# Kernel tuning notes

Measured on AMD Instinct MI355X. Metric: run time of the kernel, lower is better.

The kernel has to match this reference:

```python
import jax, jax.numpy as jnp
import numpy as np

N = 100000   # nodes
DEG = 16     # neighbors per node (uniform CSR)
E = N * DEG  # edges
D = 64       # node feature dim
COORD = 2    # coord_dim used for attention
EPS = 1e-9


def setup_inputs() -> dict:
    key = jax.random.key(0)
    k1, k2, k3, k4 = jax.random.split(key, 4)
    y = jax.random.normal(k1, (N, D), dtype=jnp.float32)
    indices = jax.random.randint(k2, (E,), 0, N, dtype=jnp.int64)
    indptr = (jnp.arange(N + 1, dtype=jnp.int64) * DEG)
    W1 = jax.random.normal(k3, (2 * D, 128), dtype=jnp.float32) * (1.0 / np.sqrt(2 * D))
    b1 = jnp.zeros((128,), dtype=jnp.float32)
    W2 = jax.random.normal(k4, (128, 64), dtype=jnp.float32) * (1.0 / np.sqrt(128))
    b2 = jnp.zeros((64,), dtype=jnp.float32)
    return {"y": y, "indices": indices, "indptr": indptr,
            "W1": W1, "b1": b1, "W2": W2, "b2": b2}


def _csr_repeat_ids(indptr, num_edges):
    # segids[e] = i such that indptr[i] <= e < indptr[i+1]
    return jnp.searchsorted(indptr, jnp.arange(num_edges, dtype=indptr.dtype), side='right') - 1


def _segment_softmax(s, segids, nsegs):
    smax = jax.ops.segment_max(s, segids, num_segments=nsegs)
    e = jnp.exp(s - smax[segids])
    denom = jax.ops.segment_sum(e, segids, num_segments=nsegs)
    return e / denom[segids]


def reference(y, indices, indptr, W1, b1, W2, b2):
    nsegs = y.shape[0]
    num_edges = indices.shape[0]
    segids = _csr_repeat_ids(indptr, num_edges)       # [E]

    rep_y = y[indices]                                # neighbor gather  [E, D]
    self_x = y[segids]                                # == repeat(x, num_reps) since x is y  [E, D]

    # cosine attention on coordinate slice
    qx = self_x[:, :COORD]
    ky = rep_y[:, :COORD]
    qn = qx / jnp.clip(jnp.linalg.norm(qx, axis=-1, keepdims=True), EPS)
    kn = ky / jnp.clip(jnp.linalg.norm(ky, axis=-1, keepdims=True), EPS)
    s = jnp.sum(qn * kn, axis=-1)                     # [E]
    a = _segment_softmax(s, segids, nsegs)            # [E]

    agg = jnp.concatenate([rep_y, self_x], axis=-1)   # [E, 2D]
    h = jax.nn.relu(agg @ W1 + b1)                    # [E, 128]
    m = h @ W2 + b2                                   # [E, 64]

    m = m * a[:, None]
    out = jax.ops.segment_sum(m, segids, num_segments=nsegs)  # [N, 64]
    return out
```

## Files before the change

### kernel.cpp

```cpp
#include <hip/hip_runtime.h>
#include <cstdint>

#define DEG 16
#define NNODE 100000
#define NTILE 3125
#define NT64 1563

typedef _Float16 f16;
typedef _Float16 h2v  __attribute__((ext_vector_type(2)));
typedef _Float16 f16x8 __attribute__((ext_vector_type(8)));
typedef float    f32x4 __attribute__((ext_vector_type(4)));

union U4 { uint4 u; h2v h[4]; f16x8 v; };
union U1 { uint32_t i; h2v h; };

__device__ __forceinline__ h2v pk2h(float a, float b) {
    auto r = __builtin_amdgcn_cvt_pkrtz(a, b);
    h2v o;
    __builtin_memcpy(&o, &r, sizeof(o));
    return o;
}

__device__ __host__ __forceinline__ int kperm(int p) {
    return (p & 0xC3) | ((p & 0x0C) << 2) | ((p & 0x30) >> 2);
}

__global__ __launch_bounds__(256) void k_prep(
    const float* __restrict__ W1, const float* __restrict__ W2,
    f16* __restrict__ W1A, f16* __restrict__ W2A)
{
    const int g0 = blockIdx.x * 256 + threadIdx.x;
    for (int i = g0; i < 16384 + 8192; i += 24 * 256) {
        if (i < 16384) {
            const int j = i & 7, lane = (i >> 3) & 63, kb = (i >> 9) & 1, mt = i >> 10;
            const int m = 16 * mt + (lane & 15);
            const int k = kb * 32 + (lane >> 4) * 8 + j;
            const int row = (m < 128) ? k : (64 + k);
            const int col = m & 127;
            W1A[i] = (f16)W1[row * 128 + col];
        } else {
            const int ii = i - 16384;
            const int j = ii & 7, lane = (ii >> 3) & 63, kb = (ii >> 9) & 3, mt = ii >> 11;
            const int c = 16 * mt + (lane & 15);
            const int p = kb * 32 + (lane >> 4) * 8 + j;
            W2A[ii] = (f16)W2[kperm(p) * 64 + c];
        }
    }
}

__global__ __launch_bounds__(256, 4) void k_uv(
    const float* __restrict__ y, const f16* __restrict__ W1A,
    const float* __restrict__ b1,
    unsigned char* __restrict__ U8, f16* __restrict__ Vh, float2* __restrict__ QN)
{
    __shared__ float ysh[4096];
    const int t = threadIdx.x;
    const long nbase = (long)blockIdx.x * 64;
    const int lane = t & 63;
    const int w = t >> 6;
    const int c16 = lane & 15, q = lane >> 4;

    {
        const size_t max4 = (size_t)NNODE * 16;
        char* yb = (char*)ysh;
        #pragma unroll
        for (int i = 0; i < 4; ++i) {
            const int e = t + i * 256;
            size_t gidx = (size_t)blockIdx.x * 1024 + e;
            if (gidx >= max4) gidx = max4 - 1;
            const float4 v = ((const float4*)y)[gidx];
            const int B = e * 16;
            const int row = B >> 8;
            *(float4*)(yb + (B ^ ((row & 7) << 4))) = v;
        }
    }

    if (QN != nullptr && t < 64) {
        const long node = nbase + t;
        if (node < NNODE) {
            const float qx = y[node * 64], qy = y[node * 64 + 1];
            const float n = fmaxf(sqrtf(qx * qx + qy * qy), 1e-9f);
            QN[node] = make_float2(qx / n, qy / n);
        }
    }
    __syncthreads();

    const char* yb = (const char*)ysh;
    f16x8 bf[4][2];
    #pragma unroll
    for (int nt = 0; nt < 4; ++nt) {
        const int r = 16 * nt + c16;
        const int sw = (r & 7) << 4;
        #pragma unroll
        for (int kb = 0; kb < 2; ++kb) {
            const int base = r * 256 + kb * 128 + q * 32;
            const float4 a = *(const float4*)(yb + (base ^ sw));
            const float4 b = *(const float4*)(yb + ((base + 16) ^ sw));
            U4 rg;
            rg.h[0] = pk2h(a.x, a.y);
            rg.h[1] = pk2h(a.z, a.w);
            rg.h[2] = pk2h(b.x, b.y);
            rg.h[3] = pk2h(b.z, b.w);
            bf[nt][kb] = rg.v;
        }
    }

    f32x4 acc[4][4];
    #pragma unroll
    for (int i = 0; i < 4; ++i)
        #pragma unroll
        for (int nt = 0; nt < 4; ++nt)
            acc[i][nt] = (f32x4){0.f, 0.f, 0.f, 0.f};

    #pragma unroll
    for (int i = 0; i < 4; ++i) {
        const int mt = 4 * w + i;
        #pragma unroll
        for (int kb = 0; kb < 2; ++kb) {
            const f16x8 af = *(const f16x8*)&W1A[((mt * 2 + kb) * 64 + lane) * 8];
            #pragma unroll
            for (int nt = 0; nt < 4; ++nt)
                acc[i][nt] = __builtin_amdgcn_mfma_f32_16x16x32_f16(af, bf[nt][kb], acc[i][nt], 0, 0, 0);
        }
    }

    const bool isV = (w >= 2);
    const int wef = w & 1;
    float4 b1v[4];
    #pragma unroll
    for (int i = 0; i < 4; ++i) b1v[i] = make_float4(0.f, 0.f, 0.f, 0.f);
    if (isV) {
        #pragma unroll
        for (int i = 0; i < 4; ++i)
            b1v[i] = *(const float4*)&b1[wef * 64 + 16 * i + 4 * q];
    }

    #pragma unroll
    for (int nt = 0; nt < 4; ++nt) {
        const long node = nbase + 16 * nt + c16;
        if (node >= NNODE) continue;
        if (!isV) {
            uint4 pkt;
            uint32_t wd[4];
            #pragma unroll
            for (int i = 0; i < 4; ++i) {
                uint32_t v0 = __builtin_amdgcn_cvt_pk_fp8_f32(acc[i][nt][0], acc[i][nt][1], 0, false);
                wd[i] = __builtin_amdgcn_cvt_pk_fp8_f32(acc[i][nt][2], acc[i][nt][3], v0, true);
            }
            pkt.x = wd[0]; pkt.y = wd[1]; pkt.z = wd[2]; pkt.w = wd[3];
            *(uint4*)(U8 + node * 128 + wef * 64 + q * 16) = pkt;
        } else {
            f16* dst = Vh + node * 128 + wef * 64 + q * 16;
            U4 p0, p1;
            p0.h[0] = pk2h(acc[0][nt][0] + b1v[0].x, acc[0][nt][1] + b1v[0].y);
            p0.h[1] = pk2h(acc[0][nt][2] + b1v[0].z, acc[0][nt][3] + b1v[0].w);
            p0.h[2] = pk2h(acc[1][nt][0] + b1v[1].x, acc[1][nt][1] + b1v[1].y);
            p0.h[3] = pk2h(acc[1][nt][2] + b1v[1].z, acc[1][nt][3] + b1v[1].w);
            p1.h[0] = pk2h(acc[2][nt][0] + b1v[2].x, acc[2][nt][1] + b1v[2].y);
            p1.h[1] = pk2h(acc[2][nt][2] + b1v[2].z, acc[2][nt][3] + b1v[2].w);
            p1.h[2] = pk2h(acc[3][nt][0] + b1v[3].x, acc[3][nt][1] + b1v[3].y);
            p1.h[3] = pk2h(acc[3][nt][2] + b1v[3].z, acc[3][nt][3] + b1v[3].w);
            *(uint4*)dst       = p0.u;
            *(uint4*)(dst + 8) = p1.u;
        }
    }
}

template<bool USE_QN>
__global__ __launch_bounds__(256, 6) void k_agg(
    const float* __restrict__ y, const int* __restrict__ idx,
    const unsigned char* __restrict__ U8, const f16* __restrict__ Vh,
    const float2* __restrict__ QN, const f16* __restrict__ W2A,
    const float* __restrict__ b2, float* __restrict__ out)
{
    __shared__ uint32_t accs[8192];

    const int t = threadIdx.x, lane = t & 63, wave = t >> 6;
    const int c16 = lane & 15, quarter = lane >> 4;
    const int nodeBase = blockIdx.x * 32 + wave * 8;

    int jA[8];
    #pragma unroll
    for (int g = 0; g < 8; ++g)
        jA[g] = idx[(nodeBase + g) * DEG + c16];

    float aA[8];
    #pragma unroll
    for (int g = 0; g < 8; ++g) {
        const int i = nodeBase + g;
        float s;
        if (USE_QN) {
            const float2 qn = QN[i];
            const float2 kn = QN[jA[g]];
            s = qn.x * kn.x + qn.y * kn.y;
        } else {
            const float2 qv = *(const float2*)&y[(long)i * 64];
            const float2 kv = *(const float2*)&y[(long)jA[g] * 64];
            const float nq = fmaxf(sqrtf(qv.x * qv.x + qv.y * qv.y), 1e-9f);
            const float nk = fmaxf(sqrtf(kv.x * kv.x + kv.y * kv.y), 1e-9f);
            s = (qv.x * kv.x + qv.y * kv.y) / (nq * nk);
        }
        float m = s;
        #pragma unroll
        for (int d = 1; d < 16; d <<= 1) m = fmaxf(m, __shfl_xor(m, d));
        const float ex = __expf(s - m);
        float sum = ex;
        #pragma unroll
        for (int d = 1; d < 16; d <<= 1) sum += __shfl_xor(sum, d);
        aA[g] = ex / sum;
    }

    const uint2* Uv = (const uint2*)U8;
    const uint4* Vv = (const uint4*)Vh;
    char* accb = (char*)accs;
    char* const myTile = accb + quarter * 8192;

    uint2 ub[2][4];
    U4 vb[2];
    vb[0].u = Vv[(long)nodeBase * 16 + c16];
    #pragma unroll
    for (int ee = 0; ee < 4; ++ee) {
        const long je = __shfl(jA[0], 4 * ee + quarter);
        ub[0][ee] = Uv[je * 16 + c16];
    }

    #pragma unroll
    for (int g = 0; g < 8; ++g) {
        const int cur = g & 1, nx = cur ^ 1;
        if (g < 7) {
            vb[nx].u = Vv[(long)(nodeBase + g + 1) * 16 + c16];
            #pragma unroll
            for (int ee = 0; ee < 4; ++ee) {
                const long je = __shfl(jA[g + 1], 4 * ee + quarter);
                ub[nx][ee] = Uv[je * 16 + c16];
            }
        }
        const h2v z2 = {0, 0};
        h2v r0 = {0, 0}, r1 = {0, 0}, r2 = {0, 0}, r3 = {0, 0};
        #pragma unroll
        for (int ee = 0; ee < 4; ++ee) {
            const float ae = __shfl(aA[g], 4 * ee + quarter);
            const h2v az = pk2h(ae, ae);
            const uint2 uu = ub[cur][ee];
            auto q01 = __builtin_amdgcn_cvt_pk_f32_fp8(uu.x, false);
            auto q23 = __builtin_amdgcn_cvt_pk_f32_fp8(uu.x, true);
            auto q45 = __builtin_amdgcn_cvt_pk_f32_fp8(uu.y, false);
            auto q67 = __builtin_amdgcn_cvt_pk_f32_fp8(uu.y, true);
            const h2v u0 = pk2h(q01[0], q01[1]);
            const h2v u1 = pk2h(q23[0], q23[1]);
            const h2v u2 = pk2h(q45[0], q45[1]);
            const h2v u3 = pk2h(q67[0], q67[1]);
            r0 += __builtin_elementwise_max(u0 + vb[cur].h[0], z2) * az;
            r1 += __builtin_elementwise_max(u1 + vb[cur].h[1], z2) * az;
            r2 += __builtin_elementwise_max(u2 + vb[cur].h[2], z2) * az;
            r3 += __builtin_elementwise_max(u3 + vb[cur].h[3], z2) * az;
        }
        const int rrow = wave * 8 + g;
        U4 pk; pk.h[0] = r0; pk.h[1] = r1; pk.h[2] = r2; pk.h[3] = r3;
        *(uint4*)(myTile + ((rrow * 256 + c16 * 16) ^ ((rrow & 7) << 4))) = pk.u;
    }
    __syncthreads();

    f16x8 waf[4];
    #pragma unroll
    for (int kb = 0; kb < 4; ++kb)
        waf[kb] = *(const f16x8*)&W2A[((wave * 4 + kb) * 64 + lane) * 8];
    const float4 b2v = *(const float4*)&b2[16 * wave + quarter * 4];

    f32x4 d[2];
    #pragma unroll
    for (int nt = 0; nt < 2; ++nt) d[nt] = (f32x4){0.f, 0.f, 0.f, 0.f};
    #pragma unroll
    for (int nt = 0; nt < 2; ++nt) {
        const int n = 16 * nt + c16;
        const int sw = (n & 7) << 4;
        #pragma unroll
        for (int qt = 0; qt < 4; ++qt) {
            #pragma unroll
            for (int kb = 0; kb < 4; ++kb) {
                const f16x8 bfr = *(const f16x8*)(accb + qt * 8192 + ((n * 256 + kb * 64 + quarter * 16) ^ sw));
                d[nt] = __builtin_amdgcn_mfma_f32_16x16x32_f16(waf[kb], bfr, d[nt], 0, 0, 0);
            }
        }
    }
    #pragma unroll
    for (int nt = 0; nt < 2; ++nt) {
        const long node = blockIdx.x * 32 + 16 * nt + c16;
        const int col = 16 * wave + quarter * 4;
        float4 o;
        o.x = d[nt][0] + b2v.x; o.y = d[nt][1] + b2v.y;
        o.z = d[nt][2] + b2v.z; o.w = d[nt][3] + b2v.w;
        *(float4*)&out[node * 64 + col] = o;
    }
}

extern "C" void kernel_launch(void* const* d_in, const int* in_sizes, int n_in,
                              void* d_out, int out_size, void* d_ws, size_t ws_size,
                              hipStream_t stream) {
    const float* y   = (const float*)d_in[0];
    const int*   idx = (const int*)d_in[1];
    const float* W1  = (const float*)d_in[3];
    const float* b1  = (const float*)d_in[4];
    const float* W2  = (const float*)d_in[5];
    const float* b2  = (const float*)d_in[6];
    float* out = (float*)d_out;

    char* ws = (char*)d_ws;
    unsigned char* U8 = (unsigned char*)ws;
    f16* Vh  = (f16*)(ws + 12800000);
    f16* W1A = (f16*)(ws + 38400000);
    f16* W2A = (f16*)(ws + 38432768);
    const size_t qn_off = 38449152;
    const bool useQN = (ws_size >= qn_off + (size_t)NNODE * sizeof(float2));
    float2* QN = useQN ? (float2*)(ws + qn_off) : nullptr;

    k_prep<<<24, 256, 0, stream>>>(W1, W2, W1A, W2A);
    k_uv<<<NT64, 256, 0, stream>>>(y, W1A, b1, U8, Vh, QN);
    if (useQN)
        k_agg<true><<<NTILE, 256, 0, stream>>>(y, idx, U8, Vh, QN, W2A, b2, out);
    else
        k_agg<false><<<NTILE, 256, 0, stream>>>(y, idx, U8, Vh, nullptr, W2A, b2, out);
}
```

Before: 66.99 us.

## Reduce per-edge partials across lanes with shuffles instead of four LDS tiles

Each lane now loads 16 fp8 bytes of the U row (8 lanes per row, 8 edges per pass) instead of 8 bytes. The per-quarter partial sums are reduced within the wave using xor-shuffles before a single LDS tile is written. This shrinks shared memory from 32KB to 8KB and cuts the second-stage MFMA loop from 16 to 4 per tile, which may allow higher occupancy and fewer LDS reads. In exchange it adds 24 shuffles per node group and an extra fp16 summation order, which changes rounding.

```diff
diff --git a/kernel.cpp b/kernel.cpp
--- a/kernel.cpp
+++ b/kernel.cpp
@@ -173,10 +173,12 @@
     const float2* __restrict__ QN, const f16* __restrict__ W2A,
     const float* __restrict__ b2, float* __restrict__ out)
 {
-    __shared__ uint32_t accs[8192];
+    __shared__ uint32_t accs[2048];
 
     const int t = threadIdx.x, lane = t & 63, wave = t >> 6;
     const int c16 = lane & 15, quarter = lane >> 4;
+    const int G = lane >> 3;
+    const int c8 = lane & 7;
     const int nodeBase = blockIdx.x * 32 + wave * 8;
 
     int jA[8];
@@ -210,54 +212,80 @@
         aA[g] = ex / sum;
     }
 
-    const uint2* Uv = (const uint2*)U8;
+    const uint4* Uv = (const uint4*)U8;
     const uint4* Vv = (const uint4*)Vh;
     char* accb = (char*)accs;
-    char* const myTile = accb + quarter * 8192;
-
-    uint2 ub[2][4];
-    U4 vb[2];
-    vb[0].u = Vv[(long)nodeBase * 16 + c16];
-    #pragma unroll
-    for (int ee = 0; ee < 4; ++ee) {
-        const long je = __shfl(jA[0], 4 * ee + quarter);
-        ub[0][ee] = Uv[je * 16 + c16];
-    }
+
+    uint4 ub[2][2], vb[2][2];
+    #pragma unroll
+    for (int ee = 0; ee < 2; ++ee) {
+        const long je = __shfl(jA[0], 8 * ee + G);
+        ub[0][ee] = Uv[je * 8 + c8];
+    }
+    vb[0][0] = Vv[(long)nodeBase * 16 + c8 * 2];
+    vb[0][1] = Vv[(long)nodeBase * 16 + c8 * 2 + 1];
 
     #pragma unroll
     for (int g = 0; g < 8; ++g) {
         const int cur = g & 1, nx = cur ^ 1;
         if (g < 7) {
-            vb[nx].u = Vv[(long)(nodeBase + g + 1) * 16 + c16];
             #pragma unroll
-            for (int ee = 0; ee < 4; ++ee) {
-                const long je = __shfl(jA[g + 1], 4 * ee + quarter);
-                ub[nx][ee] = Uv[je * 16 + c16];
+            for (int ee = 0; ee < 2; ++ee) {
+                const long je = __shfl(jA[g + 1], 8 * ee + G);
+                ub[nx][ee] = Uv[je * 8 + c8];
             }
+            vb[nx][0] = Vv[(long)(nodeBase + g + 1) * 16 + c8 * 2];
+            vb[nx][1] = Vv[(long)(nodeBase + g + 1) * 16 + c8 * 2 + 1];
+        }
+        h2v vh[8];
+        {
+            U4 tv;
+            tv.u = vb[cur][0];
+            vh[0] = tv.h[0]; vh[1] = tv.h[1]; vh[2] = tv.h[2]; vh[3] = tv.h[3];
+            tv.u = vb[cur][1];
+            vh[4] = tv.h[0]; vh[5] = tv.h[1]; vh[6] = tv.h[2]; vh[7] = tv.h[3];
         }
         const h2v z2 = {0, 0};
-        h2v r0 = {0, 0}, r1 = {0, 0}, r2 = {0, 0}, r3 = {0, 0};
-        #pragma unroll
-        for (int ee = 0; ee < 4; ++ee) {
-            const float ae = __shfl(aA[g], 4 * ee + quarter);
+        h2v r[8] = {z2, z2, z2, z2, z2, z2, z2, z2};
+        #pragma unroll
+        for (int ee = 0; ee < 2; ++ee) {
+            const float ae = __shfl(aA[g], 8 * ee + G);
             const h2v az = pk2h(ae, ae);
-            const uint2 uu = ub[cur][ee];
-            auto q01 = __builtin_amdgcn_cvt_pk_f32_fp8(uu.x, false);
-            auto q23 = __builtin_amdgcn_cvt_pk_f32_fp8(uu.x, true);
-            auto q45 = __builtin_amdgcn_cvt_pk_f32_fp8(uu.y, false);
-            auto q67 = __builtin_amdgcn_cvt_pk_f32_fp8(uu.y, true);
-            const h2v u0 = pk2h(q01[0], q01[1]);
-            const h2v u1 = pk2h(q23[0], q23[1]);
-            const h2v u2 = pk2h(q45[0], q45[1]);
-            const h2v u3 = pk2h(q67[0], q67[1]);
-            r0 += __builtin_elementwise_max(u0 + vb[cur].h[0], z2) * az;
-            r1 += __builtin_elementwise_max(u1 + vb[cur].h[1], z2) * az;
-            r2 += __builtin_elementwise_max(u2 + vb[cur].h[2], z2) * az;
-            r3 += __builtin_elementwise_max(u3 + vb[cur].h[3], z2) * az;
-        }
-        const int rrow = wave * 8 + g;
-        U4 pk; pk.h[0] = r0; pk.h[1] = r1; pk.h[2] = r2; pk.h[3] = r3;
-        *(uint4*)(myTile + ((rrow * 256 + c16 * 16) ^ ((rrow & 7) << 4))) = pk.u;
+            const uint4 uu = ub[cur][ee];
+            auto p0 = __builtin_amdgcn_cvt_pk_f32_fp8(uu.x, false);
+            auto p1 = __builtin_amdgcn_cvt_pk_f32_fp8(uu.x, true);
+            auto p2 = __builtin_amdgcn_cvt_pk_f32_fp8(uu.y, false);
+            auto p3 = __builtin_amdgcn_cvt_pk_f32_fp8(uu.y, true);
+            auto p4 = __builtin_amdgcn_cvt_pk_f32_fp8(uu.z, false);
+            auto p5 = __builtin_amdgcn_cvt_pk_f32_fp8(uu.z, true);
+            auto p6 = __builtin_amdgcn_cvt_pk_f32_fp8(uu.w, false);
+            auto p7 = __builtin_amdgcn_cvt_pk_f32_fp8(uu.w, true);
+            const h2v u_[8] = {
+                pk2h(p0[0], p0[1]), pk2h(p1[0], p1[1]), pk2h(p2[0], p2[1]), pk2h(p3[0], p3[1]),
+                pk2h(p4[0], p4[1]), pk2h(p5[0], p5[1]), pk2h(p6[0], p6[1]), pk2h(p7[0], p7[1])
+            };
+            #pragma unroll
+            for (int k2 = 0; k2 < 8; ++k2)
+                r[k2] += __builtin_elementwise_max(u_[k2] + vh[k2], z2) * az;
+        }
+        #pragma unroll
+        for (int k2 = 0; k2 < 8; ++k2) {
+            U1 v; v.h = r[k2];
+            U1 o;
+            o.i = __shfl_xor(v.i, 8);  v.h = v.h + o.h;
+            o.i = __shfl_xor(v.i, 16); v.h = v.h + o.h;
+            o.i = __shfl_xor(v.i, 32); v.h = v.h + o.h;
+            r[k2] = v.h;
+        }
+        if (G == 0) {
+            const int rrow = wave * 8 + g;
+            const int sw = (rrow & 7) << 4;
+            U4 pkA, pkB;
+            pkA.h[0] = r[0]; pkA.h[1] = r[1]; pkA.h[2] = r[2]; pkA.h[3] = r[3];
+            pkB.h[0] = r[4]; pkB.h[1] = r[5]; pkB.h[2] = r[6]; pkB.h[3] = r[7];
+            *(uint4*)(accb + ((rrow * 256 + c8 * 32) ^ sw))      = pkA.u;
+            *(uint4*)(accb + ((rrow * 256 + c8 * 32 + 16) ^ sw)) = pkB.u;
+        }
     }
     __syncthreads();
 
@@ -275,12 +303,9 @@
         const int n = 16 * nt + c16;
         const int sw = (n & 7) << 4;
         #pragma unroll
-        for (int qt = 0; qt < 4; ++qt) {
-            #pragma unroll
-            for (int kb = 0; kb < 4; ++kb) {
-                const f16x8 bfr = *(const f16x8*)(accb + qt * 8192 + ((n * 256 + kb * 64 + quarter * 16) ^ sw));
-                d[nt] = __builtin_amdgcn_mfma_f32_16x16x32_f16(waf[kb], bfr, d[nt], 0, 0, 0);
-            }
+        for (int kb = 0; kb < 4; ++kb) {
+            const f16x8 bfr = *(const f16x8*)(accb + ((n * 256 + kb * 64 + quarter * 16) ^ sw));
+            d[nt] = __builtin_amdgcn_mfma_f32_16x16x32_f16(waf[kb], bfr, d[nt], 0, 0, 0);
         }
     }
     #pragma unroll
```

Result: slower. 77.21 us (+15.3%).
